# Performance work log

Measured on AMD Instinct MI355X. Metric: run time of the kernel, lower is better.

## Reference

```python
import jax, jax.numpy as jnp
import numpy as np
import math

N = 262144
D_K = 64
D_V = 64


def setup_inputs() -> dict:
    key = jax.random.key(0)
    kq, kk, kv = jax.random.split(key, 3)
    Q = jax.random.normal(kq, (N, D_K), dtype=jnp.float32)
    K = jax.random.normal(kk, (N, D_K), dtype=jnp.float32)
    V = jax.random.normal(kv, (N, D_V), dtype=jnp.float32)
    return {"Q": Q, "K": K, "V": V}


def reference(Q, K, V):
    d_k = Q.shape[-1]
    scale = 1.0 / math.sqrt(d_k)
    # rho_q: softmax over the sequence axis (dim=-2)
    q = jax.nn.softmax(Q * scale, axis=-2)  # [N, d_k]
    # rho_k: softmax over the feature axis (dim=-1)
    k = jax.nn.softmax(K * scale, axis=-1)  # [N, d_k]
    # linear attention: [d_k, d_v] context first, then project with q
    context = k.T @ V                        # [d_k, d_v]
    return q @ context                       # [N, d_v]
```

## Files before the change

### kernel.cpp

```cpp
#include <hip/hip_runtime.h>
#include <hip/hip_bf16.h>

#define NROWS 262144
#define NB1 512
#define RPB 512
#define CL 0.18033688011112042f
#define PW 20

typedef __attribute__((ext_vector_type(8))) short s8v;
typedef __attribute__((ext_vector_type(4))) short s4h;
typedef __attribute__((ext_vector_type(4))) float f4v;

__device__ __forceinline__ short f2bf(float x) {
    unsigned u = __float_as_uint(x);
    u += 0x7FFF + ((u >> 16) & 1);
    return (short)(u >> 16);
}

__device__ __forceinline__ float dpp_red16(float x) {
    int t;
    t = __builtin_amdgcn_update_dpp(0, __float_as_int(x), 0xB1,  0xF, 0xF, true);
    x += __int_as_float(t);
    t = __builtin_amdgcn_update_dpp(0, __float_as_int(x), 0x4E,  0xF, 0xF, true);
    x += __int_as_float(t);
    t = __builtin_amdgcn_update_dpp(0, __float_as_int(x), 0x141, 0xF, 0xF, true);
    x += __int_as_float(t);
    t = __builtin_amdgcn_update_dpp(0, __float_as_int(x), 0x140, 0xF, 0xF, true);
    x += __int_as_float(t);
    return x;
}

#define GL4(dst, base, OFF) \
    asm volatile("global_load_dwordx4 %0, %1, off offset:" #OFF \
                 : "=v"(dst) : "v"(base))

__global__ __launch_bounds__(256, 2) void k1_stats(const float* __restrict__ Q,
                                                   const float* __restrict__ K,
                                                   const float* __restrict__ V,
                                                   float* __restrict__ ctx_part,
                                                   float* __restrict__ qs_part)
{
    const int tid  = threadIdx.x;
    const int lane = tid & 63;
    const int wid  = tid >> 6;
    const int m    = lane & 15;
    const int g    = lane >> 4;
    const size_t base = (size_t)blockIdx.x * RPB;

    __shared__ ushort kkP[4][64][PW];
    __shared__ ushort vP [4][64][PW];
    __shared__ float  qsl[4][64];

    f4v acc[4];
#pragma unroll
    for (int va = 0; va < 4; ++va) acc[va] = f4v{0.f, 0.f, 0.f, 0.f};
    f4v qs4 = {0.f, 0.f, 0.f, 0.f};

    f4v kf[2][4], vf[2][4], qf[2][4];

#define ISSUE(CH, PB) do { \
        const float* kb = K + (base + (CH) * 64 + wid * 16 + g) * 64 + 4 * m; \
        const float* vb = V + (base + (CH) * 64 + wid * 16 + g) * 64 + 4 * m; \
        const float* qb = Q + (base + (CH) * 64 + wid * 16 + g) * 64 + 4 * m; \
        GL4(kf[PB][0], kb, 0); GL4(kf[PB][1], kb, 1024); \
        GL4(kf[PB][2], kb, 2048); GL4(kf[PB][3], kb, 3072); \
        GL4(vf[PB][0], vb, 0); GL4(vf[PB][1], vb, 1024); \
        GL4(vf[PB][2], vb, 2048); GL4(vf[PB][3], vb, 3072); \
        GL4(qf[PB][0], qb, 0); GL4(qf[PB][1], qb, 1024); \
        GL4(qf[PB][2], qb, 2048); GL4(qf[PB][3], qb, 3072); \
    } while (0)

    ISSUE(0, 0);

#pragma unroll
    for (int ch = 0; ch < 8; ++ch) {
        const int pb = ch & 1;
        if (ch < 7) {
            const int nb = (ch + 1) & 1;
            switch (ch + 1) {
                case 1: ISSUE(1, 1); break; case 2: ISSUE(2, 0); break;
                case 3: ISSUE(3, 1); break; case 4: ISSUE(4, 0); break;
                case 5: ISSUE(5, 1); break; case 6: ISSUE(6, 0); break;
                case 7: ISSUE(7, 1); break;
            }
            (void)nb;
            asm volatile("s_waitcnt vmcnt(12)" ::: "memory");
        } else {
            asm volatile("s_waitcnt vmcnt(0)" ::: "memory");
        }
        __builtin_amdgcn_sched_barrier(0);

#pragma unroll
        for (int i = 0; i < 4; ++i) {
            qs4[0] += exp2f(qf[pb][i][0] * CL); qs4[1] += exp2f(qf[pb][i][1] * CL);
            qs4[2] += exp2f(qf[pb][i][2] * CL); qs4[3] += exp2f(qf[pb][i][3] * CL);
        }
        f4v e4[4]; float rs[4];
#pragma unroll
        for (int i = 0; i < 4; ++i) {
            e4[i][0] = exp2f(kf[pb][i][0] * CL); e4[i][1] = exp2f(kf[pb][i][1] * CL);
            e4[i][2] = exp2f(kf[pb][i][2] * CL); e4[i][3] = exp2f(kf[pb][i][3] * CL);
        }
#pragma unroll
        for (int i = 0; i < 4; ++i)
            rs[i] = dpp_red16((e4[i][0] + e4[i][1]) + (e4[i][2] + e4[i][3]));
        s4h kp[4], vp4[4];
#pragma unroll
        for (int i = 0; i < 4; ++i) {
            const float inv = __builtin_amdgcn_rcpf(rs[i]);
            kp[i]  = s4h{f2bf(e4[i][0] * inv), f2bf(e4[i][1] * inv),
                         f2bf(e4[i][2] * inv), f2bf(e4[i][3] * inv)};
            vp4[i] = s4h{f2bf(vf[pb][i][0]), f2bf(vf[pb][i][1]),
                         f2bf(vf[pb][i][2]), f2bf(vf[pb][i][3])};
        }

        __syncthreads();
#pragma unroll
        for (int i = 0; i < 4; ++i) {
            const int lr = wid * 16 + i * 4 + g;
            *(s4h*)&kkP[m >> 2][lr][(m & 3) * 4] = kp[i];
            *(s4h*)&vP [m >> 2][lr][(m & 3) * 4] = vp4[i];
        }
        __syncthreads();

#pragma unroll
        for (int ks = 0; ks < 2; ++ks) {
            s8v bf;
#pragma unroll
            for (int e = 0; e < 8; ++e)
                bf[e] = (short)kkP[wid][32 * ks + 8 * g + e][m];
            s8v af[4];
#pragma unroll
            for (int va = 0; va < 4; ++va)
#pragma unroll
                for (int e = 0; e < 8; ++e)
                    af[va][e] = (short)vP[va][32 * ks + 8 * g + e][m];
#pragma unroll
            for (int va = 0; va < 4; ++va)
                acc[va] = __builtin_amdgcn_mfma_f32_16x16x32_bf16(af[va], bf, acc[va], 0, 0, 0);
        }
    }
#undef ISSUE

#pragma unroll
    for (int va = 0; va < 4; ++va)
        *(f4v*)&ctx_part[(size_t)blockIdx.x * 4096 +
                         (wid * 16 + m) * 64 + va * 16 + 4 * g] = acc[va];

#pragma unroll
    for (int c = 0; c < 4; ++c) {
        qs4[c] += __shfl_xor(qs4[c], 16);
        qs4[c] += __shfl_xor(qs4[c], 32);
    }
    if (g == 0) *(f4v*)&qsl[wid][4 * m] = qs4;
    __syncthreads();
    if (tid < 64)
        qs_part[blockIdx.x * 64 + tid] =
            (qsl[0][tid] + qsl[1][tid]) + (qsl[2][tid] + qsl[3][tid]);
}

__global__ __launch_bounds__(256) void k2(const float* __restrict__ ctx_part,
                                          const float* __restrict__ qs_part,
                                          ushort* __restrict__ ctxfT) {
    const int c = blockIdx.x;
    const int tid = threadIdx.x;
    const int bg = tid >> 4, vq = tid & 15;
    __shared__ f4v  red[16][16];
    __shared__ float qred[4][64];
    f4v s = {0.f, 0.f, 0.f, 0.f};
    for (int b = bg; b < NB1; b += 16)
        s += *(const f4v*)&ctx_part[(size_t)b * 4096 + c * 64 + vq * 4];
    float q = 0.f;
    for (int b = tid; b < NB1; b += 256) q += qs_part[b * 64 + c];
    red[bg][vq] = s;
    qred[tid >> 6][tid & 63] = q;
    __syncthreads();
    if (tid < 64) {
        float t = 0.f;
#pragma unroll
        for (int b = 0; b < 16; ++b) t += red[b][tid >> 2][tid & 3];
        float qv = (qred[0][tid] + qred[1][tid]) + (qred[2][tid] + qred[3][tid]);
        qv = dpp_red16(qv);
        qv += __shfl_xor(qv, 16);
        qv += __shfl_xor(qv, 32);
        ctxfT[tid * 64 + c] = (ushort)f2bf(t * __builtin_amdgcn_rcpf(qv));
    }
}

__global__ __launch_bounds__(256) void k3_out(const float* __restrict__ Q,
                                              const ushort* __restrict__ ctxfT,
                                              float* __restrict__ out) {
    const int tid  = threadIdx.x;
    const int lane = tid & 63;
    const int wid  = tid >> 6;
    const int li = lane & 15, g = lane >> 4;

    s8v ct[4][2];
#pragma unroll
    for (int va = 0; va < 4; ++va)
#pragma unroll
        for (int ks = 0; ks < 2; ++ks)
            ct[va][ks] = *(const s8v*)((const char*)ctxfT +
                            2 * ((va * 16 + li) * 64 + 32 * ks + 8 * g));

#pragma unroll
    for (int t = 0; t < 4; ++t) {
        const int rb  = blockIdx.x * 256 + t * 64 + wid * 16;
        const int row = rb + li;
        const f4v* qp = (const f4v*)(Q + (size_t)row * 64);
        f4v q0 = qp[2 * g], q1 = qp[2 * g + 1];
        f4v q2 = qp[8 + 2 * g], q3 = qp[8 + 2 * g + 1];
        s8v b0, b1;
#pragma unroll
        for (int e = 0; e < 4; ++e) {
            b0[e]     = f2bf(exp2f(q0[e] * CL));
            b0[e + 4] = f2bf(exp2f(q1[e] * CL));
            b1[e]     = f2bf(exp2f(q2[e] * CL));
            b1[e + 4] = f2bf(exp2f(q3[e] * CL));
        }
#pragma unroll
        for (int va = 0; va < 4; ++va) {
            f4v a = {0.f, 0.f, 0.f, 0.f};
            a = __builtin_amdgcn_mfma_f32_16x16x32_bf16(ct[va][0], b0, a, 0, 0, 0);
            a = __builtin_amdgcn_mfma_f32_16x16x32_bf16(ct[va][1], b1, a, 0, 0, 0);
            *(f4v*)&out[(size_t)row * 64 + va * 16 + 4 * g] = a;
        }
    }
}

extern "C" void kernel_launch(void* const* d_in, const int* in_sizes, int n_in,
                              void* d_out, int out_size, void* d_ws, size_t ws_size,
                              hipStream_t stream) {
    const float* Q = (const float*)d_in[0];
    const float* K = (const float*)d_in[1];
    const float* V = (const float*)d_in[2];
    float* out = (float*)d_out;

    float* w = (float*)d_ws;
    size_t off = 0;
    float*  qs_part = w + off;              off += (size_t)NB1 * 64;
    ushort* ctxfT   = (ushort*)(w + off);   off += 2048;
    float* ctx_part;
    const size_t need = (off + (size_t)NB1 * 4096) * sizeof(float);
    if (ws_size >= need) {
        ctx_part = w + off;
    } else {
        ctx_part = out;
    }

    k1_stats<<<NB1, 256, 0, stream>>>(Q, K, V, ctx_part, qs_part);
    k2<<<64, 256, 0, stream>>>(ctx_part, qs_part, ctxfT);
    k3_out<<<NROWS / 256, 256, 0, stream>>>(Q, ctxfT, out);
}
```

Measured before the change: 74.89 us.

## Cache bf16 exp(Q) in workspace during stats pass to halve Q reread

The stats kernel now also writes exp2(Q*scale) as bf16 into a workspace buffer, and the output kernel reads that bf16 tensor instead of rereading fp32 Q and recomputing the exponentials. This replaces a 64 MB fp32 read in the last pass with a 32 MB bf16 write plus a 32 MB bf16 read. The cost is extra write traffic and stores in k1. A fallback path keeps the old behaviour when the workspace is too small.

Result: slower. 79.32 us (+5.9%).

```diff
diff --git a/kernel.cpp b/kernel.cpp
--- a/kernel.cpp
+++ b/kernel.cpp
@@ -34,11 +34,13 @@
     asm volatile("global_load_dwordx4 %0, %1, off offset:" #OFF \
                  : "=v"(dst) : "v"(base))
 
+template <int USE_QT>
 __global__ __launch_bounds__(256, 2) void k1_stats(const float* __restrict__ Q,
                                                    const float* __restrict__ K,
                                                    const float* __restrict__ V,
                                                    float* __restrict__ ctx_part,
-                                                   float* __restrict__ qs_part)
+                                                   float* __restrict__ qs_part,
+                                                   ushort* __restrict__ qt)
 {
     const int tid  = threadIdx.x;
     const int lane = tid & 63;
@@ -76,14 +78,12 @@
     for (int ch = 0; ch < 8; ++ch) {
         const int pb = ch & 1;
         if (ch < 7) {
-            const int nb = (ch + 1) & 1;
             switch (ch + 1) {
                 case 1: ISSUE(1, 1); break; case 2: ISSUE(2, 0); break;
                 case 3: ISSUE(3, 1); break; case 4: ISSUE(4, 0); break;
                 case 5: ISSUE(5, 1); break; case 6: ISSUE(6, 0); break;
                 case 7: ISSUE(7, 1); break;
             }
-            (void)nb;
             asm volatile("s_waitcnt vmcnt(12)" ::: "memory");
         } else {
             asm volatile("s_waitcnt vmcnt(0)" ::: "memory");
@@ -92,8 +92,14 @@
 
 #pragma unroll
         for (int i = 0; i < 4; ++i) {
-            qs4[0] += exp2f(qf[pb][i][0] * CL); qs4[1] += exp2f(qf[pb][i][1] * CL);
-            qs4[2] += exp2f(qf[pb][i][2] * CL); qs4[3] += exp2f(qf[pb][i][3] * CL);
+            float e0 = exp2f(qf[pb][i][0] * CL), e1 = exp2f(qf[pb][i][1] * CL);
+            float e2 = exp2f(qf[pb][i][2] * CL), e3 = exp2f(qf[pb][i][3] * CL);
+            qs4[0] += e0; qs4[1] += e1; qs4[2] += e2; qs4[3] += e3;
+            if (USE_QT) {
+                const size_t row = base + ch * 64 + wid * 16 + 4 * i + g;
+                s4h qp4 = s4h{f2bf(e0), f2bf(e1), f2bf(e2), f2bf(e3)};
+                *(s4h*)&qt[row * 64 + 4 * m] = qp4;
+            }
         }
         f4v e4[4]; float rs[4];
 #pragma unroll
@@ -187,9 +193,9 @@
     }
 }
 
-__global__ __launch_bounds__(256) void k3_out(const float* __restrict__ Q,
-                                              const ushort* __restrict__ ctxfT,
-                                              float* __restrict__ out) {
+__global__ __launch_bounds__(256) void k3_qt(const ushort* __restrict__ qt,
+                                             const ushort* __restrict__ ctxfT,
+                                             float* __restrict__ out) {
     const int tid  = threadIdx.x;
     const int lane = tid & 63;
     const int wid  = tid >> 6;
@@ -205,8 +211,38 @@
 
 #pragma unroll
     for (int t = 0; t < 4; ++t) {
-        const int rb  = blockIdx.x * 256 + t * 64 + wid * 16;
-        const int row = rb + li;
+        const int row = blockIdx.x * 256 + t * 64 + wid * 16 + li;
+        const s8v b0 = *(const s8v*)&qt[(size_t)row * 64 + 8 * g];
+        const s8v b1 = *(const s8v*)&qt[(size_t)row * 64 + 32 + 8 * g];
+#pragma unroll
+        for (int va = 0; va < 4; ++va) {
+            f4v a = {0.f, 0.f, 0.f, 0.f};
+            a = __builtin_amdgcn_mfma_f32_16x16x32_bf16(ct[va][0], b0, a, 0, 0, 0);
+            a = __builtin_amdgcn_mfma_f32_16x16x32_bf16(ct[va][1], b1, a, 0, 0, 0);
+            *(f4v*)&out[(size_t)row * 64 + va * 16 + 4 * g] = a;
+        }
+    }
+}
+
+__global__ __launch_bounds__(256) void k3_q(const float* __restrict__ Q,
+                                            const ushort* __restrict__ ctxfT,
+                                            float* __restrict__ out) {
+    const int tid  = threadIdx.x;
+    const int lane = tid & 63;
+    const int wid  = tid >> 6;
+    const int li = lane & 15, g = lane >> 4;
+
+    s8v ct[4][2];
+#pragma unroll
+    for (int va = 0; va < 4; ++va)
+#pragma unroll
+        for (int ks = 0; ks < 2; ++ks)
+            ct[va][ks] = *(const s8v*)((const char*)ctxfT +
+                            2 * ((va * 16 + li) * 64 + 32 * ks + 8 * g));
+
+#pragma unroll
+    for (int t = 0; t < 4; ++t) {
+        const int row = blockIdx.x * 256 + t * 64 + wid * 16 + li;
         const f4v* qp = (const f4v*)(Q + (size_t)row * 64);
         f4v q0 = qp[2 * g], q1 = qp[2 * g + 1];
         f4v q2 = qp[8 + 2 * g], q3 = qp[8 + 2 * g + 1];
@@ -240,15 +276,25 @@
     size_t off = 0;
     float*  qs_part = w + off;              off += (size_t)NB1 * 64;
     ushort* ctxfT   = (ushort*)(w + off);   off += 2048;
+    const size_t off_fixed = off;
+
     float* ctx_part;
-    const size_t need = (off + (size_t)NB1 * 4096) * sizeof(float);
-    if (ws_size >= need) {
-        ctx_part = w + off;
+    size_t off2 = off_fixed;
+    const size_t need_ctx = (off_fixed + (size_t)NB1 * 4096) * sizeof(float);
+    if (ws_size >= need_ctx) { ctx_part = w + off2; off2 += (size_t)NB1 * 4096; }
+    else                     { ctx_part = out; }
+
+    const size_t qt_floats = (size_t)NROWS * 64 / 2;
+    const int use_qt = (ws_size >= (off2 + qt_floats) * sizeof(float)) ? 1 : 0;
+    ushort* qt = (ushort*)(w + off2);
+
+    if (use_qt) {
+        k1_stats<1><<<NB1, 256, 0, stream>>>(Q, K, V, ctx_part, qs_part, qt);
+        k2<<<64, 256, 0, stream>>>(ctx_part, qs_part, ctxfT);
+        k3_qt<<<NROWS / 256, 256, 0, stream>>>(qt, ctxfT, out);
     } else {
-        ctx_part = out;
-    }
-
-    k1_stats<<<NB1, 256, 0, stream>>>(Q, K, V, ctx_part, qs_part);
-    k2<<<64, 256, 0, stream>>>(ctx_part, qs_part, ctxfT);
-    k3_out<<<NROWS / 256, 256, 0, stream>>>(Q, ctxfT, out);
-}
+        k1_stats<0><<<NB1, 256, 0, stream>>>(Q, K, V, ctx_part, qs_part, qt);
+        k2<<<64, 256, 0, stream>>>(ctx_part, qs_part, ctxfT);
+        k3_q<<<NROWS / 256, 256, 0, stream>>>(Q, ctxfT, out);
+    }
+}
```

## Use 512-thread blocks in stats kernel, splitting MFMA output tiles across eight waves

Applied to the files above, without the earlier changes.

The stats kernel now runs 8 waves per block instead of 4. Each chunk covers 128 rows, so the loop runs 4 iterations instead of 8. Each wave computes only two of the 16x16 output tiles (one K column block times two V column blocks) across 4 k-steps, where before it computed four tiles across 2 k-steps. The aim is more memory-level parallelism and occupancy per CU, which should help latency-hide the streaming loads. The cost is doubled LDS use per block and more synchronisation among waves.

New measurement: 82.90 us. 1.11x slower.

```diff
diff --git a/kernel.cpp b/kernel.cpp
--- a/kernel.cpp
+++ b/kernel.cpp
@@ -34,7 +34,7 @@
     asm volatile("global_load_dwordx4 %0, %1, off offset:" #OFF \
                  : "=v"(dst) : "v"(base))
 
-__global__ __launch_bounds__(256, 2) void k1_stats(const float* __restrict__ Q,
+__global__ __launch_bounds__(512, 4) void k1_stats(const float* __restrict__ Q,
                                                    const float* __restrict__ K,
                                                    const float* __restrict__ V,
                                                    float* __restrict__ ctx_part,
@@ -45,23 +45,24 @@
     const int wid  = tid >> 6;
     const int m    = lane & 15;
     const int g    = lane >> 4;
+    const int cb   = wid >> 1;
+    const int vb0  = (wid & 1) * 2;
     const size_t base = (size_t)blockIdx.x * RPB;
 
-    __shared__ ushort kkP[4][64][PW];
-    __shared__ ushort vP [4][64][PW];
-    __shared__ float  qsl[4][64];
-
-    f4v acc[4];
-#pragma unroll
-    for (int va = 0; va < 4; ++va) acc[va] = f4v{0.f, 0.f, 0.f, 0.f};
-    f4v qs4 = {0.f, 0.f, 0.f, 0.f};
+    __shared__ ushort kkP[4][128][PW];
+    __shared__ ushort vP [4][128][PW];
+    __shared__ float  qsl[8][64];
+
+    f4v acc0 = {0.f, 0.f, 0.f, 0.f};
+    f4v acc1 = {0.f, 0.f, 0.f, 0.f};
+    f4v qs4  = {0.f, 0.f, 0.f, 0.f};
 
     f4v kf[2][4], vf[2][4], qf[2][4];
 
 #define ISSUE(CH, PB) do { \
-        const float* kb = K + (base + (CH) * 64 + wid * 16 + g) * 64 + 4 * m; \
-        const float* vb = V + (base + (CH) * 64 + wid * 16 + g) * 64 + 4 * m; \
-        const float* qb = Q + (base + (CH) * 64 + wid * 16 + g) * 64 + 4 * m; \
+        const float* kb = K + (base + (CH) * 128 + wid * 16 + g) * 64 + 4 * m; \
+        const float* vb = V + (base + (CH) * 128 + wid * 16 + g) * 64 + 4 * m; \
+        const float* qb = Q + (base + (CH) * 128 + wid * 16 + g) * 64 + 4 * m; \
         GL4(kf[PB][0], kb, 0); GL4(kf[PB][1], kb, 1024); \
         GL4(kf[PB][2], kb, 2048); GL4(kf[PB][3], kb, 3072); \
         GL4(vf[PB][0], vb, 0); GL4(vf[PB][1], vb, 1024); \
@@ -73,17 +74,14 @@
     ISSUE(0, 0);
 
 #pragma unroll
-    for (int ch = 0; ch < 8; ++ch) {
+    for (int ch = 0; ch < 4; ++ch) {
         const int pb = ch & 1;
-        if (ch < 7) {
-            const int nb = (ch + 1) & 1;
+        if (ch < 3) {
             switch (ch + 1) {
-                case 1: ISSUE(1, 1); break; case 2: ISSUE(2, 0); break;
-                case 3: ISSUE(3, 1); break; case 4: ISSUE(4, 0); break;
-                case 5: ISSUE(5, 1); break; case 6: ISSUE(6, 0); break;
-                case 7: ISSUE(7, 1); break;
+                case 1: ISSUE(1, 1); break;
+                case 2: ISSUE(2, 0); break;
+                case 3: ISSUE(3, 1); break;
             }
-            (void)nb;
             asm volatile("s_waitcnt vmcnt(12)" ::: "memory");
         } else {
             asm volatile("s_waitcnt vmcnt(0)" ::: "memory");
@@ -124,28 +122,24 @@
         __syncthreads();
 
 #pragma unroll
-        for (int ks = 0; ks < 2; ++ks) {
-            s8v bf;
-#pragma unroll
-            for (int e = 0; e < 8; ++e)
-                bf[e] = (short)kkP[wid][32 * ks + 8 * g + e][m];
-            s8v af[4];
-#pragma unroll
-            for (int va = 0; va < 4; ++va)
-#pragma unroll
-                for (int e = 0; e < 8; ++e)
-                    af[va][e] = (short)vP[va][32 * ks + 8 * g + e][m];
-#pragma unroll
-            for (int va = 0; va < 4; ++va)
-                acc[va] = __builtin_amdgcn_mfma_f32_16x16x32_bf16(af[va], bf, acc[va], 0, 0, 0);
+        for (int ks = 0; ks < 4; ++ks) {
+            s8v bf, af0, af1;
+#pragma unroll
+            for (int e = 0; e < 8; ++e) {
+                bf[e]  = (short)kkP[cb][32 * ks + 8 * g + e][m];
+                af0[e] = (short)vP[vb0][32 * ks + 8 * g + e][m];
+                af1[e] = (short)vP[vb0 + 1][32 * ks + 8 * g + e][m];
+            }
+            acc0 = __builtin_amdgcn_mfma_f32_16x16x32_bf16(af0, bf, acc0, 0, 0, 0);
+            acc1 = __builtin_amdgcn_mfma_f32_16x16x32_bf16(af1, bf, acc1, 0, 0, 0);
         }
     }
 #undef ISSUE
 
-#pragma unroll
-    for (int va = 0; va < 4; ++va)
-        *(f4v*)&ctx_part[(size_t)blockIdx.x * 4096 +
-                         (wid * 16 + m) * 64 + va * 16 + 4 * g] = acc[va];
+    *(f4v*)&ctx_part[(size_t)blockIdx.x * 4096 +
+                     (cb * 16 + m) * 64 + vb0 * 16 + 4 * g]       = acc0;
+    *(f4v*)&ctx_part[(size_t)blockIdx.x * 4096 +
+                     (cb * 16 + m) * 64 + (vb0 + 1) * 16 + 4 * g] = acc1;
 
 #pragma unroll
     for (int c = 0; c < 4; ++c) {
@@ -154,9 +148,12 @@
     }
     if (g == 0) *(f4v*)&qsl[wid][4 * m] = qs4;
     __syncthreads();
-    if (tid < 64)
-        qs_part[blockIdx.x * 64 + tid] =
-            (qsl[0][tid] + qsl[1][tid]) + (qsl[2][tid] + qsl[3][tid]);
+    if (tid < 64) {
+        float s = 0.f;
+#pragma unroll
+        for (int w = 0; w < 8; ++w) s += qsl[w][tid];
+        qs_part[blockIdx.x * 64 + tid] = s;
+    }
 }
 
 __global__ __launch_bounds__(256) void k2(const float* __restrict__ ctx_part,
@@ -205,8 +202,7 @@
 
 #pragma unroll
     for (int t = 0; t < 4; ++t) {
-        const int rb  = blockIdx.x * 256 + t * 64 + wid * 16;
-        const int row = rb + li;
+        const int row = blockIdx.x * 256 + t * 64 + wid * 16 + li;
         const f4v* qp = (const f4v*)(Q + (size_t)row * 64);
         f4v q0 = qp[2 * g], q1 = qp[2 * g + 1];
         f4v q2 = qp[8 + 2 * g], q3 = qp[8 + 2 * g + 1];
@@ -248,7 +244,7 @@
         ctx_part = out;
     }
 
-    k1_stats<<<NB1, 256, 0, stream>>>(Q, K, V, ctx_part, qs_part);
+    k1_stats<<<NB1, 512, 0, stream>>>(Q, K, V, ctx_part, qs_part);
     k2<<<64, 256, 0, stream>>>(ctx_part, qs_part, ctxfT);
     k3_out<<<NROWS / 256, 256, 0, stream>>>(Q, ctxfT, out);
 }
```
